# Performance work log

Measured on AMD Instinct MI355X. Metric: run time of the kernel, lower is better.

## Reference

```python
import jax, jax.numpy as jnp
import numpy as np

N, L, K, D = 16, 1024, 1024, 1024

def setup_inputs() -> dict:
    key = jax.random.key(0)
    k1, k2, k3, k4 = jax.random.split(key, 4)
    scale = 1.0 / np.sqrt(D)
    return {
        "a1": jax.random.normal(k1, (N, L, D), dtype=jnp.float32),
        "a2": jax.random.normal(k2, (N, K, D), dtype=jnp.float32),
        "G_w": jax.random.normal(k3, (D, D), dtype=jnp.float32) * scale,
        "G_b": jax.random.normal(k4, (D,), dtype=jnp.float32) * scale,
    }

def reference(a1, a2, G_w, G_b):
    # Eval mode: LockedDropout is identity. att_type == 0.
    a2p = jnp.einsum('nkd,ed->nke', a2, G_w) + G_b       # G(a2): n,K,d
    S = jnp.einsum('nld,nkd->nlk', a1, a2p)              # score: n,L,K
    A1 = jax.nn.softmax(S, axis=2)                       # over K
    A2 = jax.nn.softmax(S, axis=1)                       # over L
    M1 = jnp.einsum('nlk,nkd->nld', A1, a2)              # n,L,d
    M2 = jnp.einsum('nlk,nld->nkd', A2, a1)              # n,K,d (A2^T @ a1)
    return (M1, M2)
```

## Files before the change

kernel.cpp:

```cpp
#include <hip/hip_runtime.h>
#include <stdint.h>

#define DEVI __device__ __forceinline__

typedef __attribute__((ext_vector_type(4))) float f32x4;
typedef __attribute__((ext_vector_type(8))) short bf16x8;
typedef __attribute__((ext_vector_type(4))) unsigned short u16x4;

DEVI unsigned short f2bf(float x) {
  union { float f; uint32_t u; } v; v.f = x;
  uint32_t r = v.u + 0x7FFFu + ((v.u >> 16) & 1u);
  return (unsigned short)(r >> 16);
}
DEVI float bf2f(unsigned short h) {
  union { uint32_t u; float f; } v; v.u = ((uint32_t)h) << 16;
  return v.f;
}

DEVI void async16(const void* g, void* l) {
  __builtin_amdgcn_global_load_lds((__attribute__((address_space(1))) void*)g,
                                   (__attribute__((address_space(3))) void*)l,
                                   16, 0, 0);
}

__global__ void k_split2(const float* __restrict__ x0, unsigned short* __restrict__ h0,
                         unsigned short* __restrict__ l0,
                         const float* __restrict__ x1, unsigned short* __restrict__ h1,
                         unsigned short* __restrict__ l1) {
  const long i = (long)blockIdx.x * 256 + threadIdx.x;
  const float* x = blockIdx.y ? x1 : x0;
  unsigned short* hh = blockIdx.y ? h1 : h0;
  unsigned short* ll = blockIdx.y ? l1 : l0;
  const f32x4 v = ((const f32x4*)x)[i];
  u16x4 H, L;
#pragma unroll
  for (int j = 0; j < 4; ++j) {
    H[j] = f2bf(v[j]);
    L[j] = f2bf(v[j] - bf2f(H[j]));
  }
  ((u16x4*)hh)[i] = H;
  ((u16x4*)ll)[i] = L;
}

__global__ void k_split(const float* __restrict__ x, unsigned short* __restrict__ hi,
                        unsigned short* __restrict__ lo, const long n4) {
  const long i = (long)blockIdx.x * 256 + threadIdx.x;
  if (i >= n4) return;
  const f32x4 v = ((const f32x4*)x)[i];
  u16x4 H, L;
#pragma unroll
  for (int j = 0; j < 4; ++j) {
    H[j] = f2bf(v[j]);
    L[j] = f2bf(v[j] - bf2f(H[j]));
  }
  ((u16x4*)hi)[i] = H;
  ((u16x4*)lo)[i] = L;
}

template<bool SPLIT, bool OUTSPLIT, bool DUAL>
__global__ __launch_bounds__(512, 2)
void k_gemm256(const unsigned short* __restrict__ Ah, const unsigned short* __restrict__ Al,
               const unsigned short* __restrict__ Bh, const unsigned short* __restrict__ Bl,
               const float* __restrict__ bias,
               float* __restrict__ Cf, unsigned short* __restrict__ Ch,
               unsigned short* __restrict__ Cl,
               const unsigned short* __restrict__ Ax, const unsigned short* __restrict__ Bx,
               float* __restrict__ Cx,
               const int Kd, const int Nn,
               const long sA, const long sB, const long sC,
               const int lgx, const int lgy) {
  __shared__ __align__(16) unsigned short smem[65536];
  const int tid  = threadIdx.x;
  const int lane = tid & 63;
  const int wave = tid >> 6;
  const int wm = wave >> 2, wn = wave & 3;
  const int m16 = lane & 15, quad = lane >> 4;

  const int nper = (int)gridDim.x >> 3;
  const int lin = (int)blockIdx.x;
  const int wg = (lin & 7) * nper + (lin >> 3);
  const int by = wg & ((1 << lgy) - 1);
  const int bx = (wg >> lgy) & ((1 << lgx) - 1);
  int bz = wg >> (lgx + lgy);

  const unsigned short* Ap = Ah;
  const unsigned short* Bp = Bh;
  float* Cp = Cf;
  if (DUAL && bz >= 16) { Ap = Ax; Bp = Bx; Cp = Cx; bz -= 16; }

  const long aTile = (long)bz * sA + (long)bx * 256 * Kd;
  const long bTile = (long)bz * sB + (long)by * 256 * Kd;

  const int row = tid & 255;
  const int kg  = tid >> 8;
  const long aoff = aTile + (long)row * Kd + kg * 8;
  const long boff = bTile + (long)row * Kd + kg * 8;

  const unsigned short* gA0 = Ap + aoff;
  const unsigned short* gA1 = SPLIT ? (Al + aoff) : (Ap + aoff + 32);
  const unsigned short* gB0 = Bp + boff;
  const unsigned short* gB1 = SPLIT ? (Bl + boff) : (Bp + boff + 32);

  const int ldsA0 = (wave >> 2) * 2048 + (wave & 3) * 512;
  const int ldsA1 = ldsA0 + 8192;
  const int ldsB0 = ldsA0 + 16384;
  const int ldsB1 = ldsA0 + 24576;

  auto STAGE = [&](int bufb, int koff) {
    async16(gA0 + koff,      smem + bufb + ldsA0);
    async16(gA0 + koff + 16, smem + bufb + ldsA0 + 4096);
    async16(gA1 + koff,      smem + bufb + ldsA1);
    async16(gA1 + koff + 16, smem + bufb + ldsA1 + 4096);
    async16(gB0 + koff,      smem + bufb + ldsB0);
    async16(gB0 + koff + 16, smem + bufb + ldsB0 + 4096);
    async16(gB1 + koff,      smem + bufb + ldsB1);
    async16(gB1 + koff + 16, smem + bufb + ldsB1 + 4096);
  };

  f32x4 acc[8][4];
#pragma unroll
  for (int i = 0; i < 8; ++i)
#pragma unroll
    for (int j = 0; j < 4; ++j) acc[i][j] = (f32x4){0.0f, 0.0f, 0.0f, 0.0f};

  const int KSTEP = SPLIT ? 32 : 64;
  const int NT = Kd / KSTEP;

  STAGE(0, 0);
  STAGE(32768, KSTEP);

  const int arow = wm * 128 + m16;
  const int brow = wn * 64 + m16;

  int kt = 2 * KSTEP;
  for (int i = 0; i < NT; ++i) {
    const int bufb = (i & 1) << 15;
    if (i + 1 < NT) asm volatile("s_waitcnt vmcnt(8)" ::: "memory");
    else            asm volatile("s_waitcnt vmcnt(0)" ::: "memory");
    asm volatile("s_barrier" ::: "memory");

    const bf16x8* fA0 = (const bf16x8*)(smem + bufb);
    const bf16x8* fA1 = (const bf16x8*)(smem + bufb + 8192);
    const bf16x8* fB0 = (const bf16x8*)(smem + bufb + 16384);
    const bf16x8* fB1 = (const bf16x8*)(smem + bufb + 24576);

    bf16x8 b0[4], b1[4];
#pragma unroll
    for (int tn = 0; tn < 4; ++tn) {
      b0[tn] = fB0[quad * 256 + brow + tn * 16];
      b1[tn] = fB1[quad * 256 + brow + tn * 16];
    }
    bf16x8 aF0[4], aF1[4];
#pragma unroll
    for (int t = 0; t < 4; ++t) {
      aF0[t] = fA0[quad * 256 + arow + t * 16];
      aF1[t] = fA1[quad * 256 + arow + t * 16];
    }
    __builtin_amdgcn_s_setprio(1);
#pragma unroll
    for (int tm = 0; tm < 4; ++tm)
#pragma unroll
      for (int tn = 0; tn < 4; ++tn) {
        acc[tm][tn] = __builtin_amdgcn_mfma_f32_16x16x32_bf16(aF0[tm], b0[tn], acc[tm][tn], 0, 0, 0);
        if (SPLIT) {
          acc[tm][tn] = __builtin_amdgcn_mfma_f32_16x16x32_bf16(aF0[tm], b1[tn], acc[tm][tn], 0, 0, 0);
          acc[tm][tn] = __builtin_amdgcn_mfma_f32_16x16x32_bf16(aF1[tm], b0[tn], acc[tm][tn], 0, 0, 0);
        } else {
          acc[tm][tn] = __builtin_amdgcn_mfma_f32_16x16x32_bf16(aF1[tm], b1[tn], acc[tm][tn], 0, 0, 0);
        }
      }
    __builtin_amdgcn_s_setprio(0);
    bf16x8 aS0[4], aS1[4];
#pragma unroll
    for (int t = 0; t < 4; ++t) {
      aS0[t] = fA0[quad * 256 + arow + (t + 4) * 16];
      aS1[t] = fA1[quad * 256 + arow + (t + 4) * 16];
    }
    asm volatile("s_waitcnt lgkmcnt(0)" ::: "memory");
    __builtin_amdgcn_sched_barrier(0);
    asm volatile("s_barrier" ::: "memory");
    if (i + 2 < NT) { STAGE(bufb, kt); kt += KSTEP; }
    __builtin_amdgcn_s_setprio(1);
#pragma unroll
    for (int tm = 0; tm < 4; ++tm)
#pragma unroll
      for (int tn = 0; tn < 4; ++tn) {
        acc[tm + 4][tn] = __builtin_amdgcn_mfma_f32_16x16x32_bf16(aS0[tm], b0[tn], acc[tm + 4][tn], 0, 0, 0);
        if (SPLIT) {
          acc[tm + 4][tn] = __builtin_amdgcn_mfma_f32_16x16x32_bf16(aS0[tm], b1[tn], acc[tm + 4][tn], 0, 0, 0);
          acc[tm + 4][tn] = __builtin_amdgcn_mfma_f32_16x16x32_bf16(aS1[tm], b0[tn], acc[tm + 4][tn], 0, 0, 0);
        } else {
          acc[tm + 4][tn] = __builtin_amdgcn_mfma_f32_16x16x32_bf16(aS1[tm], b1[tn], acc[tm + 4][tn], 0, 0, 0);
        }
      }
    __builtin_amdgcn_s_setprio(0);
  }

  const long crow0 = (long)bx * 256 + wm * 128;
  const long ccol0 = (long)by * 256 + wn * 64;
  const long cBase = (long)bz * sC;
#pragma unroll
  for (int tn = 0; tn < 4; ++tn) {
    const long gcol = ccol0 + tn * 16 + m16;
    const float bv = OUTSPLIT ? bias[gcol] : 0.0f;
#pragma unroll
    for (int tm = 0; tm < 8; ++tm) {
#pragma unroll
      for (int r = 0; r < 4; ++r) {
        const long grow = crow0 + tm * 16 + quad * 4 + r;
        const long idx = cBase + grow * (long)Nn + gcol;
        const float val = acc[tm][tn][r] + bv;
        if (OUTSPLIT) {
          unsigned short h = f2bf(val);
          Ch[idx] = h;
          Cl[idx] = f2bf(val - bf2f(h));
        } else {
          Cp[idx] = val;
        }
      }
    }
  }
}

__global__ void k_rcstats(const float* __restrict__ S, float* __restrict__ m1,
                          float* __restrict__ r1, float* __restrict__ mp,
                          float* __restrict__ sp) {
  if (blockIdx.x < 4096) {
    const int lane = threadIdx.x & 63;
    const int wave = threadIdx.x >> 6;
    const long row = (long)blockIdx.x * 4 + wave;
    const f32x4* p = (const f32x4*)(S + (row << 10));
    f32x4 v[4];
#pragma unroll
    for (int j = 0; j < 4; ++j) v[j] = p[lane + j * 64];
    float mx = -3.4e38f;
#pragma unroll
    for (int j = 0; j < 4; ++j)
#pragma unroll
      for (int c = 0; c < 4; ++c) mx = fmaxf(mx, v[j][c]);
#pragma unroll
    for (int off = 32; off > 0; off >>= 1) mx = fmaxf(mx, __shfl_xor(mx, off, 64));
    float s = 0.0f;
#pragma unroll
    for (int j = 0; j < 4; ++j)
#pragma unroll
      for (int c = 0; c < 4; ++c) s += __expf(v[j][c] - mx);
#pragma unroll
    for (int off = 32; off > 0; off >>= 1) s += __shfl_xor(s, off, 64);
    if (lane == 0) { m1[row] = mx; r1[row] = 1.0f / s; }
  } else {
    const int b = blockIdx.x - 4096;
    const int kc = b & 3, lc = (b >> 2) & 3, n = b >> 4;
    const int k = kc * 256 + threadIdx.x;
    const float* p = S + ((long)n << 20) + ((long)(lc * 256) << 10) + k;
    float m = -3.4e38f, s = 0.0f;
    for (int i = 0; i < 256; ++i) {
      const float x = p[(long)i << 10];
      const float nm = fmaxf(m, x);
      s = s * __expf(m - nm) + __expf(x - nm);
      m = nm;
    }
    const long o = ((long)(n * 4 + lc) << 10) + k;
    mp[o] = m; sp[o] = s;
  }
}

__global__ void k_colstats_comb(const float* __restrict__ mp, const float* __restrict__ sp,
                                float* __restrict__ m2, float* __restrict__ r2) {
  const int n = blockIdx.y;
  const int k = blockIdx.x * 256 + threadIdx.x;
  float m = -3.4e38f, s = 0.0f;
#pragma unroll
  for (int c = 0; c < 4; ++c) {
    const long o = ((long)(n * 4 + c) << 10) + k;
    const float mc = mp[o], sc = sp[o];
    const float nm = fmaxf(m, mc);
    s = s * __expf(m - nm) + sc * __expf(mc - nm);
    m = nm;
  }
  m2[((long)n << 10) + k] = m;
  r2[((long)n << 10) + k] = 1.0f / s;
}

__global__ void k_agen(const float* __restrict__ S, const float* __restrict__ m1,
                       const float* __restrict__ r1, const float* __restrict__ m2,
                       const float* __restrict__ r2, unsigned short* __restrict__ A1,
                       unsigned short* __restrict__ A2T) {
  __shared__ float e2[64][65];
  const int n = blockIdx.z;
  const int k0 = blockIdx.x * 64, l0 = blockIdx.y * 64;
  const int q = threadIdx.x >> 4, p = threadIdx.x & 15;
  const long nb = (long)n << 20;
  const int kk = k0 + p * 4;
  const f32x4 mm2 = *(const f32x4*)(m2 + ((long)n << 10) + kk);
  const f32x4 rr2 = *(const f32x4*)(r2 + ((long)n << 10) + kk);
#pragma unroll
  for (int rr = 0; rr < 4; ++rr) {
    const int lrow = rr * 16 + q;
    const int l = l0 + lrow;
    const f32x4 s4 = *(const f32x4*)(S + nb + ((long)l << 10) + kk);
    const float mv = m1[((long)n << 10) + l], rv = r1[((long)n << 10) + l];
    u16x4 o;
#pragma unroll
    for (int j = 0; j < 4; ++j) {
      o[j] = f2bf(__expf(s4[j] - mv) * rv);
      e2[lrow][p * 4 + j] = __expf(s4[j] - mm2[j]) * rr2[j];
    }
    *(u16x4*)(A1 + nb + ((long)l << 10) + kk) = o;
  }
  __syncthreads();
#pragma unroll
  for (int rr = 0; rr < 4; ++rr) {
    const int krow = rr * 16 + q;
    u16x4 o;
#pragma unroll
    for (int j = 0; j < 4; ++j) o[j] = f2bf(e2[p * 4 + j][krow]);
    *(u16x4*)(A2T + nb + ((long)(k0 + krow) << 10) + (l0 + p * 4)) = o;
  }
}

__global__ void k_transpose2(const float* __restrict__ in0, unsigned short* __restrict__ out0,
                             const float* __restrict__ in1, unsigned short* __restrict__ out1) {
  __shared__ float t[64][65];
  const int zz = blockIdx.z;
  const int n = zz & 15;
  const float* in = (zz < 16) ? in0 : in1;
  unsigned short* out = (zz < 16) ? out0 : out1;
  const int c0 = blockIdx.x * 64, r0 = blockIdx.y * 64;
  const int q = threadIdx.x >> 4, p = threadIdx.x & 15;
  const long nb = (long)n << 20;
#pragma unroll
  for (int rr = 0; rr < 4; ++rr) {
    const int r = rr * 16 + q;
    const f32x4 v = *(const f32x4*)(in + nb + ((long)(r0 + r) << 10) + c0 + p * 4);
#pragma unroll
    for (int j = 0; j < 4; ++j) t[r][p * 4 + j] = v[j];
  }
  __syncthreads();
#pragma unroll
  for (int rr = 0; rr < 4; ++rr) {
    const int c = rr * 16 + q;
    u16x4 o;
#pragma unroll
    for (int j = 0; j < 4; ++j) o[j] = f2bf(t[p * 4 + j][c]);
    *(u16x4*)(out + nb + ((long)(c0 + c) << 10) + (r0 + p * 4)) = o;
  }
}

extern "C" void kernel_launch(void* const* d_in, const int* in_sizes, int n_in,
                              void* d_out, int out_size, void* d_ws, size_t ws_size,
                              hipStream_t stream) {
  const float* a1 = (const float*)d_in[0];
  const float* a2 = (const float*)d_in[1];
  const float* Gw = (const float*)d_in[2];
  const float* Gb = (const float*)d_in[3];
  float* out = (float*)d_out;
  char* ws = (char*)d_ws;
  const size_t MB = 1ull << 20;

  unsigned short* a1h  = (unsigned short*)(ws + 0 * MB);
  unsigned short* a1l  = (unsigned short*)(ws + 32 * MB);
  unsigned short* a2h  = (unsigned short*)(ws + 64 * MB);
  unsigned short* a2l  = (unsigned short*)(ws + 96 * MB);
  unsigned short* a2ph = (unsigned short*)(ws + 128 * MB);
  unsigned short* a2pl = (unsigned short*)(ws + 160 * MB);
  unsigned short* Gh   = (unsigned short*)(ws + 192 * MB);
  unsigned short* Gl   = (unsigned short*)(ws + 194 * MB);
  char* st = ws + 196 * MB;
  float* m1 = (float*)(st);
  float* r1 = (float*)(st + 64 * 1024);
  float* m2 = (float*)(st + 128 * 1024);
  float* r2 = (float*)(st + 192 * 1024);
  float* mp = (float*)(st + 256 * 1024);
  float* sp = (float*)(st + 512 * 1024);
  float* S            = (float*)(ws + 64 * MB);
  unsigned short* A1  = (unsigned short*)(ws + 0 * MB);
  unsigned short* A2T = (unsigned short*)(ws + 32 * MB);
  unsigned short* a2T = (unsigned short*)(ws + 128 * MB);
  unsigned short* a1T = (unsigned short*)(ws + 160 * MB);

  const long B1M = 1048576;

  k_split2<<<dim3(16384, 2), 256, 0, stream>>>(a1, a1h, a1l, a2, a2h, a2l);
  k_split<<<1024, 256, 0, stream>>>(Gw, Gh, Gl, 262144);

  k_gemm256<true, true, false><<<256, 512, 0, stream>>>(
      a2h, a2l, Gh, Gl, Gb, nullptr, a2ph, a2pl, nullptr, nullptr, nullptr,
      1024, 1024, 0, 0, 0, 6, 2);

  k_gemm256<true, false, false><<<256, 512, 0, stream>>>(
      a1h, a1l, a2ph, a2pl, nullptr, S, nullptr, nullptr, nullptr, nullptr, nullptr,
      1024, 1024, B1M, B1M, B1M, 2, 2);

  k_rcstats<<<4352, 256, 0, stream>>>(S, m1, r1, mp, sp);
  k_colstats_comb<<<dim3(4, 16), 256, 0, stream>>>(mp, sp, m2, r2);

  k_agen<<<dim3(16, 16, 16), 256, 0, stream>>>(S, m1, r1, m2, r2, A1, A2T);

  k_transpose2<<<dim3(16, 16, 32), 256, 0, stream>>>(a2, a2T, a1, a1T);

  k_gemm256<false, false, true><<<512, 512, 0, stream>>>(
      A1, nullptr, a2T, nullptr, nullptr, out, nullptr, nullptr,
      A2T, a1T, out + 16777216,
      1024, 1024, B1M, B1M, B1M, 2, 2);
}
```

Measured before the change: 727.8 us.

## Split GEMM main loop into four phases interleaving async loads with MFMA

Restructures the bf16 GEMM mainloop from two halves into four MFMA phases. Each phase issues a slice of the next tile's global-to-LDS async loads: the A halves go into the other buffer, and the B halves go into the current buffer two steps ahead, since B is already held in registers. The aim is to spread memory traffic evenly across compute and keep the MFMA pipe busy, in the style of ping-pong schedules. The cost is more barriers per iteration and tricky vmcnt/lgkmcnt accounting, which risks stalls or races if the counts are wrong.

```diff
diff --git a/kernel.cpp b/kernel.cpp
--- a/kernel.cpp
+++ b/kernel.cpp
@@ -101,21 +101,7 @@
   const unsigned short* gB0 = Bp + boff;
   const unsigned short* gB1 = SPLIT ? (Bl + boff) : (Bp + boff + 32);
 
-  const int ldsA0 = (wave >> 2) * 2048 + (wave & 3) * 512;
-  const int ldsA1 = ldsA0 + 8192;
-  const int ldsB0 = ldsA0 + 16384;
-  const int ldsB1 = ldsA0 + 24576;
-
-  auto STAGE = [&](int bufb, int koff) {
-    async16(gA0 + koff,      smem + bufb + ldsA0);
-    async16(gA0 + koff + 16, smem + bufb + ldsA0 + 4096);
-    async16(gA1 + koff,      smem + bufb + ldsA1);
-    async16(gA1 + koff + 16, smem + bufb + ldsA1 + 4096);
-    async16(gB0 + koff,      smem + bufb + ldsB0);
-    async16(gB0 + koff + 16, smem + bufb + ldsB0 + 4096);
-    async16(gB1 + koff,      smem + bufb + ldsB1);
-    async16(gB1 + koff + 16, smem + bufb + ldsB1 + 4096);
-  };
+  const int ldsW = (wave >> 2) * 2048 + (wave & 3) * 512;
 
   f32x4 acc[8][4];
 #pragma unroll
@@ -126,75 +112,131 @@
   const int KSTEP = SPLIT ? 32 : 64;
   const int NT = Kd / KSTEP;
 
-  STAGE(0, 0);
-  STAGE(32768, KSTEP);
-
-  const int arow = wm * 128 + m16;
-  const int brow = wn * 64 + m16;
-
-  int kt = 2 * KSTEP;
+  async16(gA0,              smem + ldsW);
+  async16(gA0 + 16,         smem + ldsW + 4096);
+  async16(gA1,              smem + 8192 + ldsW);
+  async16(gA1 + 16,         smem + 8192 + ldsW + 4096);
+  async16(gB0,              smem + 16384 + ldsW);
+  async16(gB0 + 16,         smem + 16384 + ldsW + 4096);
+  async16(gB1,              smem + 24576 + ldsW);
+  async16(gB1 + 16,         smem + 24576 + ldsW + 4096);
+  async16(gB0 + KSTEP,      smem + 32768 + 16384 + ldsW);
+  async16(gB0 + KSTEP + 16, smem + 32768 + 16384 + ldsW + 4096);
+  async16(gB1 + KSTEP,      smem + 32768 + 24576 + ldsW);
+  async16(gB1 + KSTEP + 16, smem + 32768 + 24576 + ldsW + 4096);
+  asm volatile("s_waitcnt vmcnt(4)" ::: "memory");
+  asm volatile("s_barrier" ::: "memory");
+
+  const int abase = quad * 256 + wm * 128 + m16;
+  const int bbase = quad * 256 + wn * 64 + m16;
+
+#define MFMA_PHASE(q, A0, A1)                                                               \
+  {                                                                                         \
+    _Pragma("unroll")                                                                       \
+    for (int j = 0; j < 2; ++j) {                                                           \
+      _Pragma("unroll")                                                                     \
+      for (int tn = 0; tn < 4; ++tn) {                                                      \
+        acc[2*(q)+j][tn] = __builtin_amdgcn_mfma_f32_16x16x32_bf16(A0[j], b0[tn],           \
+                                                                   acc[2*(q)+j][tn], 0,0,0);\
+        if (SPLIT) {                                                                        \
+          acc[2*(q)+j][tn] = __builtin_amdgcn_mfma_f32_16x16x32_bf16(A0[j], b1[tn],         \
+                                                                   acc[2*(q)+j][tn], 0,0,0);\
+          acc[2*(q)+j][tn] = __builtin_amdgcn_mfma_f32_16x16x32_bf16(A1[j], b0[tn],         \
+                                                                   acc[2*(q)+j][tn], 0,0,0);\
+        } else {                                                                            \
+          acc[2*(q)+j][tn] = __builtin_amdgcn_mfma_f32_16x16x32_bf16(A1[j], b1[tn],         \
+                                                                   acc[2*(q)+j][tn], 0,0,0);\
+        }                                                                                   \
+      }                                                                                     \
+    }                                                                                       \
+  }
+
   for (int i = 0; i < NT; ++i) {
-    const int bufb = (i & 1) << 15;
-    if (i + 1 < NT) asm volatile("s_waitcnt vmcnt(8)" ::: "memory");
-    else            asm volatile("s_waitcnt vmcnt(0)" ::: "memory");
-    asm volatile("s_barrier" ::: "memory");
-
-    const bf16x8* fA0 = (const bf16x8*)(smem + bufb);
-    const bf16x8* fA1 = (const bf16x8*)(smem + bufb + 8192);
-    const bf16x8* fB0 = (const bf16x8*)(smem + bufb + 16384);
-    const bf16x8* fB1 = (const bf16x8*)(smem + bufb + 24576);
+    const int cur = (i & 1) << 15;
+    const int nxt = cur ^ 32768;
+    const bf16x8* fA0 = (const bf16x8*)(smem + cur);
+    const bf16x8* fA1 = (const bf16x8*)(smem + cur + 8192);
+    const bf16x8* fB0 = (const bf16x8*)(smem + cur + 16384);
+    const bf16x8* fB1 = (const bf16x8*)(smem + cur + 24576);
+    const int kA = (i + 1) * KSTEP;
+    const int kB = (i + 2) * KSTEP;
+    const bool stA = (i + 1 < NT), stB = (i + 2 < NT);
 
     bf16x8 b0[4], b1[4];
-#pragma unroll
-    for (int tn = 0; tn < 4; ++tn) {
-      b0[tn] = fB0[quad * 256 + brow + tn * 16];
-      b1[tn] = fB1[quad * 256 + brow + tn * 16];
-    }
-    bf16x8 aF0[4], aF1[4];
-#pragma unroll
-    for (int t = 0; t < 4; ++t) {
-      aF0[t] = fA0[quad * 256 + arow + t * 16];
-      aF1[t] = fA1[quad * 256 + arow + t * 16];
-    }
-    __builtin_amdgcn_s_setprio(1);
-#pragma unroll
-    for (int tm = 0; tm < 4; ++tm)
+    {
 #pragma unroll
       for (int tn = 0; tn < 4; ++tn) {
-        acc[tm][tn] = __builtin_amdgcn_mfma_f32_16x16x32_bf16(aF0[tm], b0[tn], acc[tm][tn], 0, 0, 0);
-        if (SPLIT) {
-          acc[tm][tn] = __builtin_amdgcn_mfma_f32_16x16x32_bf16(aF0[tm], b1[tn], acc[tm][tn], 0, 0, 0);
-          acc[tm][tn] = __builtin_amdgcn_mfma_f32_16x16x32_bf16(aF1[tm], b0[tn], acc[tm][tn], 0, 0, 0);
-        } else {
-          acc[tm][tn] = __builtin_amdgcn_mfma_f32_16x16x32_bf16(aF1[tm], b1[tn], acc[tm][tn], 0, 0, 0);
-        }
-      }
-    __builtin_amdgcn_s_setprio(0);
-    bf16x8 aS0[4], aS1[4];
-#pragma unroll
-    for (int t = 0; t < 4; ++t) {
-      aS0[t] = fA0[quad * 256 + arow + (t + 4) * 16];
-      aS1[t] = fA1[quad * 256 + arow + (t + 4) * 16];
-    }
-    asm volatile("s_waitcnt lgkmcnt(0)" ::: "memory");
-    __builtin_amdgcn_sched_barrier(0);
-    asm volatile("s_barrier" ::: "memory");
-    if (i + 2 < NT) { STAGE(bufb, kt); kt += KSTEP; }
-    __builtin_amdgcn_s_setprio(1);
-#pragma unroll
-    for (int tm = 0; tm < 4; ++tm)
-#pragma unroll
-      for (int tn = 0; tn < 4; ++tn) {
-        acc[tm + 4][tn] = __builtin_amdgcn_mfma_f32_16x16x32_bf16(aS0[tm], b0[tn], acc[tm + 4][tn], 0, 0, 0);
-        if (SPLIT) {
-          acc[tm + 4][tn] = __builtin_amdgcn_mfma_f32_16x16x32_bf16(aS0[tm], b1[tn], acc[tm + 4][tn], 0, 0, 0);
-          acc[tm + 4][tn] = __builtin_amdgcn_mfma_f32_16x16x32_bf16(aS1[tm], b0[tn], acc[tm + 4][tn], 0, 0, 0);
-        } else {
-          acc[tm + 4][tn] = __builtin_amdgcn_mfma_f32_16x16x32_bf16(aS1[tm], b1[tn], acc[tm + 4][tn], 0, 0, 0);
-        }
-      }
-    __builtin_amdgcn_s_setprio(0);
-  }
+        b0[tn] = fB0[bbase + tn * 16];
+        b1[tn] = fB1[bbase + tn * 16];
+      }
+      bf16x8 a0[2], a1[2];
+      a0[0] = fA0[abase];      a0[1] = fA0[abase + 16];
+      a1[0] = fA1[abase];      a1[1] = fA1[abase + 16];
+      if (stA) {
+        async16(gA0 + kA,      smem + nxt + ldsW);
+        async16(gA0 + kA + 16, smem + nxt + ldsW + 4096);
+      }
+      asm volatile("s_waitcnt lgkmcnt(8)" ::: "memory");
+      asm volatile("s_barrier" ::: "memory");
+      asm volatile("s_waitcnt lgkmcnt(0)" ::: "memory");
+      __builtin_amdgcn_sched_barrier(0);
+      __builtin_amdgcn_s_setprio(1);
+      MFMA_PHASE(0, a0, a1);
+      __builtin_amdgcn_s_setprio(0);
+      asm volatile("s_barrier" ::: "memory");
+    }
+    {
+      bf16x8 a0[2], a1[2];
+      a0[0] = fA0[abase + 32]; a0[1] = fA0[abase + 48];
+      a1[0] = fA1[abase + 32]; a1[1] = fA1[abase + 48];
+      if (stA) {
+        async16(gA1 + kA,      smem + nxt + 8192 + ldsW);
+        async16(gA1 + kA + 16, smem + nxt + 8192 + ldsW + 4096);
+      }
+      asm volatile("s_barrier" ::: "memory");
+      asm volatile("s_waitcnt lgkmcnt(0)" ::: "memory");
+      __builtin_amdgcn_sched_barrier(0);
+      __builtin_amdgcn_s_setprio(1);
+      MFMA_PHASE(1, a0, a1);
+      __builtin_amdgcn_s_setprio(0);
+      asm volatile("s_barrier" ::: "memory");
+    }
+    {
+      bf16x8 a0[2], a1[2];
+      a0[0] = fA0[abase + 64]; a0[1] = fA0[abase + 80];
+      a1[0] = fA1[abase + 64]; a1[1] = fA1[abase + 80];
+      if (stB) {
+        async16(gB0 + kB,      smem + cur + 16384 + ldsW);
+        async16(gB0 + kB + 16, smem + cur + 16384 + ldsW + 4096);
+      }
+      asm volatile("s_barrier" ::: "memory");
+      asm volatile("s_waitcnt lgkmcnt(0)" ::: "memory");
+      __builtin_amdgcn_sched_barrier(0);
+      __builtin_amdgcn_s_setprio(1);
+      MFMA_PHASE(2, a0, a1);
+      __builtin_amdgcn_s_setprio(0);
+      asm volatile("s_barrier" ::: "memory");
+    }
+    {
+      bf16x8 a0[2], a1[2];
+      a0[0] = fA0[abase + 96];  a0[1] = fA0[abase + 112];
+      a1[0] = fA1[abase + 96];  a1[1] = fA1[abase + 112];
+      if (stB) {
+        async16(gB1 + kB,      smem + cur + 24576 + ldsW);
+        async16(gB1 + kB + 16, smem + cur + 24576 + ldsW + 4096);
+      }
+      asm volatile("s_barrier" ::: "memory");
+      asm volatile("s_waitcnt lgkmcnt(0)" ::: "memory");
+      __builtin_amdgcn_sched_barrier(0);
+      __builtin_amdgcn_s_setprio(1);
+      MFMA_PHASE(3, a0, a1);
+      __builtin_amdgcn_s_setprio(0);
+      if (stB) asm volatile("s_waitcnt vmcnt(4)" ::: "memory");
+      else     asm volatile("s_waitcnt vmcnt(0)" ::: "memory");
+      asm volatile("s_barrier" ::: "memory");
+    }
+  }
+#undef MFMA_PHASE
 
   const long crow0 = (long)bx * 256 + wm * 128;
   const long ccol0 = (long)by * 256 + wn * 64;
```

Result: faster. 652.8 us (-10.3%).
